# Performance work log

Hardware: AMD Instinct MI355X
Metric: run time of the kernel (lower is better)

## Reference

```python
import jax, jax.numpy as jnp
import numpy as np

D_MODEL = 1024
NUM_HEADS = 16
HEAD_DIM = D_MODEL // NUM_HEADS
SEQ_LEN = 2048
BATCH = 2
THETA = 10000.0


def apply_rope(x, token_positions):
    # x: (..., seq, head_dim); token_positions: (seq,)
    d_k = x.shape[-1]
    inv_freq = 1.0 / (THETA ** (jnp.arange(0, d_k, 2, dtype=jnp.float32) / d_k))  # (d_k/2,)
    angle = token_positions.astype(jnp.float32)[:, None] * inv_freq[None, :]       # (seq, d_k/2)
    cos, sin = jnp.cos(angle), jnp.sin(angle)
    xr = x.reshape(*x.shape[:-1], d_k // 2, 2)
    a, b = xr[..., 0], xr[..., 1]  # real, imag parts of consecutive pairs
    # complex multiply (a + ib) * (cos + i sin)
    out_r = a * cos - b * sin
    out_i = a * sin + b * cos
    return jnp.stack([out_r, out_i], axis=-1).reshape(x.shape)


def setup_inputs() -> dict:
    key = jax.random.key(0)
    ks = jax.random.split(key, 5)
    std = np.sqrt(2.0 / (D_MODEL + D_MODEL))
    return {
        "x": jax.random.normal(ks[0], (BATCH, SEQ_LEN, D_MODEL), dtype=jnp.float32),
        "Wq": jax.random.normal(ks[1], (D_MODEL, D_MODEL), dtype=jnp.float32) * std,
        "Wk": jax.random.normal(ks[2], (D_MODEL, D_MODEL), dtype=jnp.float32) * std,
        "Wv": jax.random.normal(ks[3], (D_MODEL, D_MODEL), dtype=jnp.float32) * std,
        "Wo": jax.random.normal(ks[4], (D_MODEL, D_MODEL), dtype=jnp.float32) * std,
        "token_positions": jnp.arange(SEQ_LEN, dtype=jnp.int32),
    }


def reference(x, Wq, Wk, Wv, Wo, token_positions):
    B, L, D = x.shape
    H, Dh = NUM_HEADS, HEAD_DIM

    def proj(W):  # '... d_in, d_out d_in -> ... d_out' then split heads -> (B,H,L,Dh)
        y = jnp.einsum('bld,ed->ble', x, W)
        return y.reshape(B, L, H, Dh).transpose(0, 2, 1, 3)

    q = apply_rope(proj(Wq), token_positions)
    k = apply_rope(proj(Wk), token_positions)
    v = proj(Wv)

    scores = jnp.einsum('bhqd,bhkd->bhqk', q, k) / jnp.sqrt(jnp.float32(Dh))  # (B,H,L,L)
    causal = jnp.tril(jnp.ones((L, L), dtype=bool))
    scores = jnp.where(causal, scores, -jnp.inf)
    attn = jax.nn.softmax(scores, axis=-1)
    o = jnp.einsum('bhqk,bhkd->bhqd', attn, v)  # (B,H,L,Dh)
    o = o.transpose(0, 2, 1, 3).reshape(B, L, D)
    return jnp.einsum('bld,ed->ble', o, Wo)
```

## Files before the change

kernel.cpp:

```cpp
#include <hip/hip_runtime.h>

typedef __bf16 bf16;
typedef __attribute__((ext_vector_type(8))) __bf16 bf16x8;
typedef __attribute__((ext_vector_type(4))) __bf16 bf16x4;
typedef __attribute__((ext_vector_type(4))) float f32x4;

__device__ inline bf16 f2bf(float f) {
  unsigned u = __builtin_bit_cast(unsigned, f);
  u += 0x7fff + ((u >> 16) & 1);
  unsigned short h = (unsigned short)(u >> 16);
  return __builtin_bit_cast(bf16, h);
}

__device__ inline void gl_lds16(const bf16* g, bf16* l) {
  __builtin_amdgcn_global_load_lds(
      (const __attribute__((address_space(1))) void*)g,
      (__attribute__((address_space(3))) void*)l, 16, 0, 0);
}

__global__ __launch_bounds__(256) void cvt_kernel(
    const float* __restrict__ x, const float* __restrict__ wq,
    const float* __restrict__ wk, const float* __restrict__ wv,
    const float* __restrict__ wo, bf16* __restrict__ dst,
    const int* __restrict__ pos, float* __restrict__ tab) {
  if (blockIdx.x >= 8192) {
    int gid = (blockIdx.x - 8192) * 256 + threadIdx.x;
    int tok = gid >> 5, j = gid & 31;
    float freq = exp2f(-(float)(2 * j) * 0.20762051f);
    float angle = (float)pos[tok] * freq;
    float sn, cs;
    sincosf(angle, &sn, &cs);
    *(float2*)(tab + tok * 64 + j * 2) = make_float2(cs, sn);
    return;
  }
  int idx = (blockIdx.x * 256 + threadIdx.x) * 4;
  const float* src;
  if (idx < 4194304) {
    src = x + idx;
  } else {
    int j = idx - 4194304;
    int w = j >> 20;
    const float* sw = (w == 0) ? wq : (w == 1) ? wk : (w == 2) ? wv : wo;
    src = sw + (j & 1048575);
  }
  float4 f = *(const float4*)src;
  bf16x4 o = {f2bf(f.x), f2bf(f.y), f2bf(f.z), f2bf(f.w)};
  *(bf16x4*)(dst + idx) = o;
}

__global__ __launch_bounds__(256) void gemm_qkv_kernel(
    const bf16* __restrict__ xb, const bf16* __restrict__ wb,
    const float* __restrict__ tab,
    bf16* __restrict__ Qb, bf16* __restrict__ Kb, bf16* __restrict__ Vtb) {
  __shared__ __align__(16) bf16 smem[16384];
  bf16* As = smem;
  bf16* Bs = smem + 8192;
  int tid = threadIdx.x;
  int lane = tid & 63, w = tid >> 6;
  int l15 = lane & 15, quad = lane >> 4;
  int bid = blockIdx.x;
  int sb = (bid & 7) * 96 + (bid >> 3);
  int bx = sb % 24, by = sb / 24;
  int mb = by * 128, nb = bx * 128;
  int mq = (w & 1) * 64, nq = (w >> 1) * 64;
  int gsw = (lane & 7) ^ ((lane >> 3) & 7);
  const bf16* agp = xb + (size_t)(mb + w * 32 + (lane >> 3)) * 1024 + gsw * 8;
  const bf16* bgp = wb + (size_t)(nb + w * 32 + (lane >> 3)) * 1024 + gsw * 8;
  bf16* alp = As + (w * 32) * 64;
  bf16* blp = Bs + (w * 32) * 64;
  f32x4 acc[4][4];
#pragma unroll
  for (int i = 0; i < 4; ++i)
#pragma unroll
    for (int j = 0; j < 4; ++j)
      for (int r = 0; r < 4; ++r) acc[i][j][r] = 0.f;
  for (int kt = 0; kt < 16; ++kt) {
#pragma unroll
    for (int i = 0; i < 4; ++i) {
      gl_lds16(agp + i * 8192, alp + i * 512);
      gl_lds16(bgp + i * 8192, blp + i * 512);
    }
    agp += 64; bgp += 64;
    __syncthreads();
#pragma unroll
    for (int c = 0; c < 2; ++c) {
      bf16x8 af[4], bfr[4];
      int rg = (c * 4 + quad);
#pragma unroll
      for (int mt = 0; mt < 4; ++mt)
        af[mt] = *(const bf16x8*)(As + (mq + mt * 16 + l15) * 64 + (rg ^ (l15 & 7)) * 8);
#pragma unroll
      for (int nt = 0; nt < 4; ++nt)
        bfr[nt] = *(const bf16x8*)(Bs + (nq + nt * 16 + l15) * 64 + (rg ^ (l15 & 7)) * 8);
#pragma unroll
      for (int mt = 0; mt < 4; ++mt)
#pragma unroll
        for (int nt = 0; nt < 4; ++nt)
          acc[mt][nt] = __builtin_amdgcn_mfma_f32_16x16x32_bf16(af[mt], bfr[nt], acc[mt][nt], 0, 0, 0);
    }
    __syncthreads();
  }
  int b = mb >> 11;
  int mtok = mb & 2047;
  if (bx < 16) {
    bf16* dst = (bx < 8) ? Qb : Kb;
#pragma unroll
    for (int nt = 0; nt < 4; ++nt) {
      int e = nb + nq + nt * 16 + l15;
      int d = e & 63;
      int h = (e & 1023) >> 6;
      int tbase = d & ~1;
#pragma unroll
      for (int mt = 0; mt < 4; ++mt) {
#pragma unroll
        for (int r = 0; r < 4; ++r) {
          int ltok = mtok + mq + mt * 16 + quad * 4 + r;
          float val = acc[mt][nt][r];
          float p = __shfl_xor(val, 1);
          float2 cs2 = *(const float2*)(tab + ltok * 64 + tbase);
          float outv = (e & 1) ? (p * cs2.y + val * cs2.x) : (val * cs2.x - p * cs2.y);
          dst[(size_t)(((b << 4) + h) * 2048 + ltok) * 64 + d] = f2bf(outv);
        }
      }
    }
  } else {
    bf16* T = smem;
    for (int h2 = 0; h2 < 2; ++h2) {
      if ((w >> 1) == h2) {
#pragma unroll
        for (int nt = 0; nt < 4; ++nt)
#pragma unroll
          for (int mt = 0; mt < 4; ++mt) {
            bf16x4 tv = {f2bf(acc[mt][nt][0]), f2bf(acc[mt][nt][1]),
                         f2bf(acc[mt][nt][2]), f2bf(acc[mt][nt][3])};
            *(bf16x4*)&T[(nt * 16 + l15) * 136 + mq + mt * 16 + quad * 4] = tv;
          }
      }
      __syncthreads();
      int row = tid >> 2, cs = (tid & 3) * 32;
      int e = nb + h2 * 64 + row;
      int d = e & 63, hh = (e & 1023) >> 6;
      bf16* vdst = Vtb + ((size_t)((b << 4) + hh) * 64 + d) * 2048 + mtok + cs;
#pragma unroll
      for (int j = 0; j < 4; ++j)
        *(bf16x8*)(vdst + j * 8) = *(const bf16x8*)&T[row * 136 + cs + j * 8];
      __syncthreads();
    }
  }
}

#define SCALE_L2E 0.18033688f
__global__ __launch_bounds__(256) void attn_kernel(
    const bf16* __restrict__ Qb, const bf16* __restrict__ Kb,
    const bf16* __restrict__ Vtb, bf16* __restrict__ Ob) {
  __shared__ __align__(16) bf16 Ks[64 * 64];
  __shared__ __align__(16) bf16 Vs[64 * 64];
  __shared__ __align__(16) bf16 pbuf[4][16 * 72];
  int tid = threadIdx.x;
  int lane = tid & 63, w = tid >> 6;
  int l15 = lane & 15, quad = lane >> 4;
  int bidx = blockIdx.x;
  int bh = bidx & 31;
  int qt = 31 - (bidx >> 5);
  int qbase = qt * 64;
  const bf16* Qp = Qb + (size_t)bh * 131072;
  const bf16* Kp = Kb + (size_t)bh * 131072;
  const bf16* Vp = Vtb + (size_t)bh * 131072;
  int r8 = lane >> 3;
  int gsw8 = (lane & 7) ^ r8;
  int g0 = quad ^ (l15 & 7);
  int g1 = (4 + quad) ^ (l15 & 7);
  bf16x8 qf[2];
#pragma unroll
  for (int c = 0; c < 2; ++c)
    qf[c] = *(const bf16x8*)(Qp + (size_t)(qbase + w * 16 + l15) * 64 + c * 32 + quad * 8);
  f32x4 oacc[4];
#pragma unroll
  for (int dt = 0; dt < 4; ++dt)
    for (int r = 0; r < 4; ++r) oacc[dt][r] = 0.f;
  float lpart = 0.f;
  int qmin_w = qbase + w * 16;
  int qmax_w = qmin_w + 15;
  int ntiles = qt + 1;

  for (int t = 0; t < ntiles; ++t) {
    int kb = t * 64;
    {
      const bf16* ksrc = Kp + (size_t)(kb + w * 16 + r8) * 64 + gsw8 * 8;
      bf16* kdst = &Ks[(w * 16) * 64];
      gl_lds16(ksrc, kdst);
      gl_lds16(ksrc + 8 * 64, kdst + 8 * 64);
      const bf16* vsrc = Vp + (size_t)(w * 16 + r8) * 2048 + kb + gsw8 * 8;
      bf16* vdst = &Vs[(w * 16) * 64];
      gl_lds16(vsrc, vdst);
      gl_lds16(vsrc + 8 * 2048, vdst + 8 * 64);
    }
    __syncthreads();
    if (kb <= qmax_w) {
      bf16x8 kf[4][2], vf[4][2];
#pragma unroll
      for (int kt = 0; kt < 4; ++kt) {
        kf[kt][0] = *(const bf16x8*)(&Ks[(kt * 16 + l15) * 64 + g0 * 8]);
        kf[kt][1] = *(const bf16x8*)(&Ks[(kt * 16 + l15) * 64 + g1 * 8]);
      }
#pragma unroll
      for (int dt = 0; dt < 4; ++dt) {
        vf[dt][0] = *(const bf16x8*)(&Vs[(dt * 16 + l15) * 64 + g0 * 8]);
        vf[dt][1] = *(const bf16x8*)(&Vs[(dt * 16 + l15) * 64 + g1 * 8]);
      }
      int q = qmin_w + l15;
      f32x4 s[4];
#pragma unroll
      for (int kt = 0; kt < 4; ++kt) {
        for (int r = 0; r < 4; ++r) s[kt][r] = 0.f;
        s[kt] = __builtin_amdgcn_mfma_f32_16x16x32_bf16(kf[kt][0], qf[0], s[kt], 0, 0, 0);
        s[kt] = __builtin_amdgcn_mfma_f32_16x16x32_bf16(kf[kt][1], qf[1], s[kt], 0, 0, 0);
      }
      float pe[16];
      if (kb + 63 > qmin_w) {
#pragma unroll
        for (int kt = 0; kt < 4; ++kt)
#pragma unroll
          for (int r = 0; r < 4; ++r) {
            int key = kb + kt * 16 + quad * 4 + r;
            pe[kt * 4 + r] = (key <= q) ? exp2f(s[kt][r] * SCALE_L2E) : 0.f;
          }
      } else {
#pragma unroll
        for (int kt = 0; kt < 4; ++kt)
#pragma unroll
          for (int r = 0; r < 4; ++r) pe[kt * 4 + r] = exp2f(s[kt][r] * SCALE_L2E);
      }
#pragma unroll
      for (int i = 0; i < 16; ++i) lpart += pe[i];
#pragma unroll
      for (int kt = 0; kt < 4; ++kt) {
        bf16x4 pw = {f2bf(pe[kt * 4]), f2bf(pe[kt * 4 + 1]), f2bf(pe[kt * 4 + 2]), f2bf(pe[kt * 4 + 3])};
        *(bf16x4*)&pbuf[w][l15 * 72 + kt * 16 + quad * 4] = pw;
      }
      bf16x8 pb0 = *(const bf16x8*)&pbuf[w][l15 * 72 + quad * 8];
      bf16x8 pb1 = *(const bf16x8*)&pbuf[w][l15 * 72 + 32 + quad * 8];
#pragma unroll
      for (int dt = 0; dt < 4; ++dt) {
        oacc[dt] = __builtin_amdgcn_mfma_f32_16x16x32_bf16(vf[dt][0], pb0, oacc[dt], 0, 0, 0);
        oacc[dt] = __builtin_amdgcn_mfma_f32_16x16x32_bf16(vf[dt][1], pb1, oacc[dt], 0, 0, 0);
      }
    }
    __syncthreads();
  }
  float lrun = lpart;
  lrun += __shfl_xor(lrun, 16);
  lrun += __shfl_xor(lrun, 32);
  int b0 = bh >> 4, h = bh & 15;
  float inv = 1.f / lrun;
  int q = qmin_w + l15;
  bf16* obase = Ob + ((size_t)(b0 * 2048 + q)) * 1024 + h * 64;
#pragma unroll
  for (int dt = 0; dt < 4; ++dt)
#pragma unroll
    for (int r = 0; r < 4; ++r)
      obase[dt * 16 + quad * 4 + r] = f2bf(oacc[dt][r] * inv);
}

__global__ __launch_bounds__(256) void gemm_out_kernel(
    const bf16* __restrict__ Ob, const bf16* __restrict__ wob,
    float* __restrict__ out) {
  __shared__ __align__(16) bf16 As[64 * 32];
  __shared__ __align__(16) bf16 Bs[64 * 32];
  int tid = threadIdx.x;
  int lane = tid & 63, w = tid >> 6;
  int l15 = lane & 15, quad = lane >> 4;
  int mb = blockIdx.y * 64, nb = blockIdx.x * 64;
  int mq = (w & 1) * 32, nq = (w >> 1) * 32;
  const bf16* agp = Ob + (size_t)(mb + w * 16 + (lane >> 2)) * 1024 + (lane & 3) * 8;
  const bf16* bgp = wob + (size_t)(nb + w * 16 + (lane >> 2)) * 1024 + (lane & 3) * 8;
  bf16* alp = As + (w * 16) * 32;
  bf16* blp = Bs + (w * 16) * 32;
  f32x4 acc[2][2];
#pragma unroll
  for (int i = 0; i < 2; ++i)
#pragma unroll
    for (int j = 0; j < 2; ++j)
      for (int r = 0; r < 4; ++r) acc[i][j][r] = 0.f;
  for (int kt = 0; kt < 32; ++kt) {
    gl_lds16(agp, alp);
    gl_lds16(bgp, blp);
    agp += 32; bgp += 32;
    __syncthreads();
    bf16x8 af[2], bfr[2];
#pragma unroll
    for (int mt = 0; mt < 2; ++mt)
      af[mt] = *(const bf16x8*)(As + (mq + mt * 16 + l15) * 32 + quad * 8);
#pragma unroll
    for (int nt = 0; nt < 2; ++nt)
      bfr[nt] = *(const bf16x8*)(Bs + (nq + nt * 16 + l15) * 32 + quad * 8);
#pragma unroll
    for (int mt = 0; mt < 2; ++mt)
#pragma unroll
      for (int nt = 0; nt < 2; ++nt)
        acc[mt][nt] = __builtin_amdgcn_mfma_f32_16x16x32_bf16(af[mt], bfr[nt], acc[mt][nt], 0, 0, 0);
    __syncthreads();
  }
#pragma unroll
  for (int mt = 0; mt < 2; ++mt)
#pragma unroll
    for (int nt = 0; nt < 2; ++nt)
#pragma unroll
      for (int r = 0; r < 4; ++r)
        out[(size_t)(mb + mq + mt * 16 + quad * 4 + r) * 1024 + nb + nq + nt * 16 + l15] = acc[mt][nt][r];
}

extern "C" void kernel_launch(void* const* d_in, const int* in_sizes, int n_in,
                              void* d_out, int out_size, void* d_ws, size_t ws_size,
                              hipStream_t stream) {
  const float* x  = (const float*)d_in[0];
  const float* wq = (const float*)d_in[1];
  const float* wk = (const float*)d_in[2];
  const float* wv = (const float*)d_in[3];
  const float* wo = (const float*)d_in[4];
  const int* pos  = (const int*)d_in[5];
  float* out = (float*)d_out;
  bf16* wsb = (bf16*)d_ws;
  bf16* xb  = wsb;
  bf16* wb  = wsb + 4194304;
  bf16* Qb  = wsb + 8388608;
  bf16* Kb  = wsb + 12582912;
  bf16* Vtb = wsb + 16777216;
  bf16* Obf = wsb + 20971520;
  float* tab = (float*)Obf;
  hipLaunchKernelGGL(cvt_kernel, dim3(8448), dim3(256), 0, stream, x, wq, wk, wv, wo, wsb, pos, tab);
  hipLaunchKernelGGL(gemm_qkv_kernel, dim3(768), dim3(256), 0, stream, xb, wb, tab, Qb, Kb, Vtb);
  hipLaunchKernelGGL(attn_kernel, dim3(1024), dim3(256), 0, stream, Qb, Kb, Vtb, Obf);
  hipLaunchKernelGGL(gemm_out_kernel, dim3(16, 64), dim3(256), 0, stream, Obf, wb + 3 * 1048576, out);
}
```

Baseline: 203.3 us.

## Enlarge output GEMM tiles with swizzled LDS and XCD-aware block mapping

The output projection GEMM moves from 64x64 tiles with K-step 32 to 128x64 tiles with K-step 64. It uses XOR-swizzled LDS loads like the QKV GEMM, and a 1D grid remapped so each XCD works on a contiguous region. The QKV GEMM block-to-tile mapping is also changed to give each XCD an 8x12 tile patch for better L2 locality. Larger tiles cut global/LDS traffic per FLOP and halve barrier count. The cost is fewer blocks (512) and more registers per thread, which could lower occupancy.

```diff
diff --git a/kernel.cpp b/kernel.cpp
--- a/kernel.cpp
+++ b/kernel.cpp
@@ -59,8 +59,9 @@
   int lane = tid & 63, w = tid >> 6;
   int l15 = lane & 15, quad = lane >> 4;
   int bid = blockIdx.x;
-  int sb = (bid & 7) * 96 + (bid >> 3);
-  int bx = sb % 24, by = sb / 24;
+  int xcd = bid & 7, j = bid >> 3;
+  int by = (xcd & 3) * 8 + (j & 7);
+  int bx = (xcd >> 2) * 12 + (j >> 3);
   int mb = by * 128, nb = bx * 128;
   int mq = (w & 1) * 64, nq = (w >> 1) * 64;
   int gsw = (lane & 7) ^ ((lane >> 3) & 7);
@@ -72,8 +73,8 @@
 #pragma unroll
   for (int i = 0; i < 4; ++i)
 #pragma unroll
-    for (int j = 0; j < 4; ++j)
-      for (int r = 0; r < 4; ++r) acc[i][j][r] = 0.f;
+    for (int j2 = 0; j2 < 4; ++j2)
+      for (int r = 0; r < 4; ++r) acc[i][j2][r] = 0.f;
   for (int kt = 0; kt < 16; ++kt) {
 #pragma unroll
     for (int i = 0; i < 4; ++i) {
@@ -142,8 +143,8 @@
       int d = e & 63, hh = (e & 1023) >> 6;
       bf16* vdst = Vtb + ((size_t)((b << 4) + hh) * 64 + d) * 2048 + mtok + cs;
 #pragma unroll
-      for (int j = 0; j < 4; ++j)
-        *(bf16x8*)(vdst + j * 8) = *(const bf16x8*)&T[row * 136 + cs + j * 8];
+      for (int j3 = 0; j3 < 4; ++j3)
+        *(bf16x8*)(vdst + j3 * 8) = *(const bf16x8*)&T[row * 136 + cs + j3 * 8];
       __syncthreads();
     }
   }
@@ -265,44 +266,57 @@
 __global__ __launch_bounds__(256) void gemm_out_kernel(
     const bf16* __restrict__ Ob, const bf16* __restrict__ wob,
     float* __restrict__ out) {
-  __shared__ __align__(16) bf16 As[64 * 32];
-  __shared__ __align__(16) bf16 Bs[64 * 32];
+  __shared__ __align__(16) bf16 As[128 * 64];
+  __shared__ __align__(16) bf16 Bs[64 * 64];
   int tid = threadIdx.x;
   int lane = tid & 63, w = tid >> 6;
   int l15 = lane & 15, quad = lane >> 4;
-  int mb = blockIdx.y * 64, nb = blockIdx.x * 64;
-  int mq = (w & 1) * 32, nq = (w >> 1) * 32;
-  const bf16* agp = Ob + (size_t)(mb + w * 16 + (lane >> 2)) * 1024 + (lane & 3) * 8;
-  const bf16* bgp = wob + (size_t)(nb + w * 16 + (lane >> 2)) * 1024 + (lane & 3) * 8;
-  bf16* alp = As + (w * 16) * 32;
-  bf16* blp = Bs + (w * 16) * 32;
-  f32x4 acc[2][2];
-#pragma unroll
-  for (int i = 0; i < 2; ++i)
-#pragma unroll
-    for (int j = 0; j < 2; ++j)
-      for (int r = 0; r < 4; ++r) acc[i][j][r] = 0.f;
-  for (int kt = 0; kt < 32; ++kt) {
-    gl_lds16(agp, alp);
-    gl_lds16(bgp, blp);
-    agp += 32; bgp += 32;
-    __syncthreads();
-    bf16x8 af[2], bfr[2];
-#pragma unroll
-    for (int mt = 0; mt < 2; ++mt)
-      af[mt] = *(const bf16x8*)(As + (mq + mt * 16 + l15) * 32 + quad * 8);
-#pragma unroll
-    for (int nt = 0; nt < 2; ++nt)
-      bfr[nt] = *(const bf16x8*)(Bs + (nq + nt * 16 + l15) * 32 + quad * 8);
-#pragma unroll
-    for (int mt = 0; mt < 2; ++mt)
+  int bid = blockIdx.x;
+  int xcd = bid & 7, j = bid >> 3;
+  int by = (xcd & 3) * 8 + (j & 7);
+  int bx = (xcd >> 2) * 8 + (j >> 3);
+  int mb = by * 128, nb = bx * 64;
+  int mq = (w & 1) * 64, nq = (w >> 1) * 32;
+  int gsw = (lane & 7) ^ ((lane >> 3) & 7);
+  const bf16* agp = Ob + (size_t)(mb + w * 32 + (lane >> 3)) * 1024 + gsw * 8;
+  const bf16* bgp = wob + (size_t)(nb + w * 16 + (lane >> 3)) * 1024 + gsw * 8;
+  bf16* alp = As + (w * 32) * 64;
+  bf16* blp = Bs + (w * 16) * 64;
+  f32x4 acc[4][2];
+#pragma unroll
+  for (int i = 0; i < 4; ++i)
+#pragma unroll
+    for (int j2 = 0; j2 < 2; ++j2)
+      for (int r = 0; r < 4; ++r) acc[i][j2][r] = 0.f;
+  for (int kt = 0; kt < 16; ++kt) {
+#pragma unroll
+    for (int i = 0; i < 4; ++i)
+      gl_lds16(agp + i * 8192, alp + i * 512);
+#pragma unroll
+    for (int i = 0; i < 2; ++i)
+      gl_lds16(bgp + i * 8192, blp + i * 512);
+    agp += 64; bgp += 64;
+    __syncthreads();
+#pragma unroll
+    for (int c = 0; c < 2; ++c) {
+      bf16x8 af[4], bfr[2];
+      int rg = (c * 4 + quad);
+#pragma unroll
+      for (int mt = 0; mt < 4; ++mt)
+        af[mt] = *(const bf16x8*)(As + (mq + mt * 16 + l15) * 64 + (rg ^ (l15 & 7)) * 8);
 #pragma unroll
       for (int nt = 0; nt < 2; ++nt)
-        acc[mt][nt] = __builtin_amdgcn_mfma_f32_16x16x32_bf16(af[mt], bfr[nt], acc[mt][nt], 0, 0, 0);
-    __syncthreads();
-  }
-#pragma unroll
-  for (int mt = 0; mt < 2; ++mt)
+        bfr[nt] = *(const bf16x8*)(Bs + (nq + nt * 16 + l15) * 64 + (rg ^ (l15 & 7)) * 8);
+#pragma unroll
+      for (int mt = 0; mt < 4; ++mt)
+#pragma unroll
+        for (int nt = 0; nt < 2; ++nt)
+          acc[mt][nt] = __builtin_amdgcn_mfma_f32_16x16x32_bf16(af[mt], bfr[nt], acc[mt][nt], 0, 0, 0);
+    }
+    __syncthreads();
+  }
+#pragma unroll
+  for (int mt = 0; mt < 4; ++mt)
 #pragma unroll
     for (int nt = 0; nt < 2; ++nt)
 #pragma unroll
@@ -331,5 +345,5 @@
   hipLaunchKernelGGL(cvt_kernel, dim3(8448), dim3(256), 0, stream, x, wq, wk, wv, wo, wsb, pos, tab);
   hipLaunchKernelGGL(gemm_qkv_kernel, dim3(768), dim3(256), 0, stream, xb, wb, tab, Qb, Kb, Vtb);
   hipLaunchKernelGGL(attn_kernel, dim3(1024), dim3(256), 0, stream, Qb, Kb, Vtb, Obf);
-  hipLaunchKernelGGL(gemm_out_kernel, dim3(16, 64), dim3(256), 0, stream, Obf, wb + 3 * 1048576, out);
-}
+  hipLaunchKernelGGL(gemm_out_kernel, dim3(512), dim3(256), 0, stream, Obf, wb + 3 * 1048576, out);
+}
```

Result: no change. 201.7 us (-0.8%).
